# Kernel optimization log

Measured on AMD Instinct MI355X. Metric: run time of the kernel, lower is better.

Reference implementation:

```python
import jax, jax.numpy as jnp
import numpy as np

# db4 decomposition low-pass filter (pywt convention, 8 taps)
DEC_LO = np.array([-0.010597401784997278, 0.032883011666982945, 0.030841381835986965,
                   -0.18703481171888114, -0.02798376941698385, 0.6308807679295904,
                   0.7148465705525415, 0.23037781330885523], dtype=np.float32)
L = DEC_LO.shape[0]  # 8
REC_LO = DEC_LO[::-1].copy()
DEC_HI = (REC_LO * ((-1.0) ** (np.arange(L) + 1))).astype(np.float32)
REC_HI = DEC_HI[::-1].copy()
LEVEL = 7

# lax.conv does correlation; flip filters to get true convolution (pywt semantics)
K_DEC = jnp.asarray(np.stack([DEC_LO[::-1], DEC_HI[::-1]])[:, None, :])  # [2,1,L] out-ch: (lo, hi)
K_REC = jnp.asarray(np.stack([REC_LO[::-1], REC_HI[::-1]])[None, :, :])  # [1,2,L] in-ch: (ca, cd)


def dwt(x):
    # x: [B, N]. pywt zero-mode dwt == full conv then take odd indices;
    # fused here as stride-2 conv with asymmetric padding (L-2, L-1).
    y = jax.lax.conv_general_dilated(x[:, None, :], K_DEC, (2,), [(L - 2, L - 1)])
    return y[:, 0], y[:, 1]  # each [B, floor((N+L-1)/2)]


def idwt(ca, cd):
    # upsample-by-2 (lhs_dilation, length 2n-1), full conv, trim L-2 each side -> pad (1,1)
    y = jax.lax.conv_general_dilated(jnp.stack([ca, cd], axis=1), K_REC, (1,),
                                     [(1, 1)], lhs_dilation=(2,))
    return y[:, 0]  # [B, 2n - L + 2]


def soft(c, t):
    # pywt.threshold(mode='soft')
    return jnp.sign(c) * jnp.maximum(jnp.abs(c) - t, 0.0)


def setup_inputs() -> dict:
    key = jax.random.key(0)
    k1, k2 = jax.random.split(key)
    x = jax.random.normal(k1, (32768, 1116), dtype=jnp.float32)
    # learned scalar parameter, initialized like nn.Parameter(torch.tensor(0.02))
    raw_threshold = jnp.asarray(0.02, dtype=jnp.float32)
    return {"x": x, "raw_threshold": raw_threshold}


def reference(x, raw_threshold):
    thr = jnp.maximum(raw_threshold, 0.01)  # torch.clamp(min=0.01)
    # wavedec: 7-level analysis
    a = x
    details = []
    for _ in range(LEVEL):
        a, d = dwt(a)
        details.append(d)
    # soft-threshold every coefficient band (including approximation)
    a = soft(a, thr)
    details = [soft(d, thr) for d in details]
    # waverec: synthesis, truncating cA when one sample longer than cD (pywt rule)
    for d in reversed(details):
        if a.shape[-1] > d.shape[-1]:
            a = a[:, : d.shape[-1]]
        a = idwt(a, d)
    return a  # [B, 1116]
```

## Files before the change

### kernel.cpp

```cpp
#include <hip/hip_runtime.h>

#define NCOL 1116
#define NLEV 7
#define NT 256
#define RPB 4
#define ARENA 2048

static __device__ __forceinline__ float softf(float c, float t) {
    return copysignf(fmaxf(fabsf(c) - t, 0.0f), c);
}

__global__ __launch_bounds__(NT)
void wavelet_kernel(const float* __restrict__ x,
                    const float* __restrict__ thr_ptr,
                    float* __restrict__ out, int nrow) {
    constexpr float DEC_LO[8] = {-0.010597401784997278f,  0.032883011666982945f,
                                  0.030841381835986965f, -0.18703481171888114f,
                                 -0.02798376941698385f,   0.6308807679295904f,
                                  0.7148465705525415f,    0.23037781330885523f};
    constexpr float DEC_HI[8] = {-0.23037781330885523f,   0.7148465705525415f,
                                 -0.6308807679295904f,   -0.02798376941698385f,
                                  0.18703481171888114f,   0.030841381835986965f,
                                 -0.032883011666982945f, -0.010597401784997278f};
    constexpr float REC_LO[8] = { 0.23037781330885523f,   0.7148465705525415f,
                                  0.6308807679295904f,   -0.02798376941698385f,
                                 -0.18703481171888114f,   0.030841381835986965f,
                                  0.032883011666982945f, -0.010597401784997278f};
    constexpr float REC_HI[8] = {-0.010597401784997278f, -0.032883011666982945f,
                                  0.030841381835986965f,  0.18703481171888114f,
                                 -0.02798376941698385f,  -0.6308807679295904f,
                                  0.7148465705525415f,   -0.23037781330885523f};

    constexpr int alen[8] = {1116, 561, 284, 145, 76, 41, 24, 15};
    constexpr int doff[7] = {0, 562, 846, 992, 1068, 1110, 1134};

    __shared__ __align__(16) float SH[RPB * ARENA];

    const int lane = threadIdx.x & 63;
    const int wv   = threadIdx.x >> 6;
    const int row  = blockIdx.x * RPB + wv;
    if (row >= nrow) return;

    const float thr = fmaxf(thr_ptr[0], 0.01f);

    float* const arena = SH + wv * ARENA;
    float* const dpool = arena;
    float* const b8    = arena + 1156;
    float* const c8    = arena + 1732;

    {
        const float* xrow = x + (size_t)row * NCOL;
        #pragma unroll
        for (int k = 0; k < 9; ++k) {
            const int o = lane + (k << 6);
            if (o < 561) {
                float v[8];
                if (o >= 3 && o <= 557) {
                    const float2* p = (const float2*)(xrow + 2 * o - 6);
                    float2 q0 = p[0], q1 = p[1], q2 = p[2], q3 = p[3];
                    v[0] = q0.x; v[1] = q0.y; v[2] = q1.x; v[3] = q1.y;
                    v[4] = q2.x; v[5] = q2.y; v[6] = q3.x; v[7] = q3.y;
                } else {
                    #pragma unroll
                    for (int j = 0; j < 8; ++j) {
                        const int idx = 2 * o - 6 + j;
                        v[j] = (idx >= 0 && idx < NCOL) ? xrow[idx] : 0.0f;
                    }
                }
                float lo = 0.0f, hi = 0.0f;
                #pragma unroll
                for (int s = 0; s < 8; ++s) {
                    lo = fmaf(DEC_LO[s], v[7 - s], lo);
                    hi = fmaf(DEC_HI[s], v[7 - s], hi);
                }
                b8[o]    = lo;
                dpool[o] = softf(hi, thr);
            }
        }
        if (lane < 14) { const int j = lane < 6 ? lane - 6 : 555 + lane; b8[j] = 0.0f; }
        __builtin_amdgcn_wave_barrier();
    }

    #pragma unroll
    for (int l = 1; l < NLEV; ++l) {
        const int nout = alen[l + 1];
        float* const cur = (l & 1) ? b8 : c8;
        float* const nxt = (l & 1) ? c8 : b8;
        float* const dp  = dpool + doff[l];
        const int K = (nout + 63) >> 6;
        #pragma unroll
        for (int k = 0; k < K; ++k) {
            const int o = lane + (k << 6);
            if (o < nout) {
                const float2* p = (const float2*)(cur + 2 * o - 6);
                float2 q0 = p[0], q1 = p[1], q2 = p[2], q3 = p[3];
                float v[8];
                v[0] = q0.x; v[1] = q0.y; v[2] = q1.x; v[3] = q1.y;
                v[4] = q2.x; v[5] = q2.y; v[6] = q3.x; v[7] = q3.y;
                float lo = 0.0f, hi = 0.0f;
                #pragma unroll
                for (int s = 0; s < 8; ++s) {
                    lo = fmaf(DEC_LO[s], v[7 - s], lo);
                    hi = fmaf(DEC_HI[s], v[7 - s], hi);
                }
                nxt[o] = (l == NLEV - 1) ? softf(lo, thr) : lo;
                dp[o]  = softf(hi, thr);
            }
        }
        if (l < NLEV - 1 && lane < 14) {
            const int j = lane < 6 ? lane - 6 : nout + lane - 6;
            nxt[j] = 0.0f;
        }
        __builtin_amdgcn_wave_barrier();
    }

    #pragma unroll
    for (int l = NLEV - 1; l >= 1; --l) {
        const int M = alen[l + 1];
        const int npair = M - 3;
        const float* const cur = (l & 1) ? c8 : b8;
        float* const nxt       = (l & 1) ? b8 : c8;
        const float* const dp  = dpool + doff[l];
        const int KI = (((npair + 1) >> 1) + 63) >> 6;
        #pragma unroll
        for (int kk = 0; kk < KI; ++kk) {
            const int m = (lane + (kk << 6)) << 1;
            if (m < npair) {
                float ca[5], cd[5];
                #pragma unroll
                for (int j = 0; j < 5; ++j) { ca[j] = cur[m + j]; cd[j] = dp[m + j]; }
                float y0 = fmaf(REC_LO[0], ca[3], fmaf(REC_LO[2], ca[2], fmaf(REC_LO[4], ca[1], REC_LO[6] * ca[0])));
                y0 = fmaf(REC_HI[0], cd[3], fmaf(REC_HI[2], cd[2], fmaf(REC_HI[4], cd[1], fmaf(REC_HI[6], cd[0], y0))));
                float y1 = fmaf(REC_LO[1], ca[3], fmaf(REC_LO[3], ca[2], fmaf(REC_LO[5], ca[1], REC_LO[7] * ca[0])));
                y1 = fmaf(REC_HI[1], cd[3], fmaf(REC_HI[3], cd[2], fmaf(REC_HI[5], cd[1], fmaf(REC_HI[7], cd[0], y1))));
                if (m + 1 < npair) {
                    float y2 = fmaf(REC_LO[0], ca[4], fmaf(REC_LO[2], ca[3], fmaf(REC_LO[4], ca[2], REC_LO[6] * ca[1])));
                    y2 = fmaf(REC_HI[0], cd[4], fmaf(REC_HI[2], cd[3], fmaf(REC_HI[4], cd[2], fmaf(REC_HI[6], cd[1], y2))));
                    float y3 = fmaf(REC_LO[1], ca[4], fmaf(REC_LO[3], ca[3], fmaf(REC_LO[5], ca[2], REC_LO[7] * ca[1])));
                    y3 = fmaf(REC_HI[1], cd[4], fmaf(REC_HI[3], cd[3], fmaf(REC_HI[5], cd[2], fmaf(REC_HI[7], cd[1], y3))));
                    *(float4*)(nxt + 2 * m) = make_float4(y0, y1, y2, y3);
                } else {
                    nxt[2 * m]     = y0;
                    nxt[2 * m + 1] = y1;
                }
            }
        }
        __builtin_amdgcn_wave_barrier();
    }

    {
        const float* const cur = b8;
        const float* const dp  = dpool;
        float4* orow = (float4*)(out + (size_t)row * NCOL);
        #pragma unroll
        for (int kk = 0; kk < 5; ++kk) {
            const int bq = lane + (kk << 6);
            const int m = bq << 1;
            if (m < 558) {
                float ca[5], cd[5];
                #pragma unroll
                for (int j = 0; j < 5; ++j) { ca[j] = cur[m + j]; cd[j] = dp[m + j]; }
                float y0 = fmaf(REC_LO[0], ca[3], fmaf(REC_LO[2], ca[2], fmaf(REC_LO[4], ca[1], REC_LO[6] * ca[0])));
                y0 = fmaf(REC_HI[0], cd[3], fmaf(REC_HI[2], cd[2], fmaf(REC_HI[4], cd[1], fmaf(REC_HI[6], cd[0], y0))));
                float y1 = fmaf(REC_LO[1], ca[3], fmaf(REC_LO[3], ca[2], fmaf(REC_LO[5], ca[1], REC_LO[7] * ca[0])));
                y1 = fmaf(REC_HI[1], cd[3], fmaf(REC_HI[3], cd[2], fmaf(REC_HI[5], cd[1], fmaf(REC_HI[7], cd[0], y1))));
                float y2 = fmaf(REC_LO[0], ca[4], fmaf(REC_LO[2], ca[3], fmaf(REC_LO[4], ca[2], REC_LO[6] * ca[1])));
                y2 = fmaf(REC_HI[0], cd[4], fmaf(REC_HI[2], cd[3], fmaf(REC_HI[4], cd[2], fmaf(REC_HI[6], cd[1], y2))));
                float y3 = fmaf(REC_LO[1], ca[4], fmaf(REC_LO[3], ca[3], fmaf(REC_LO[5], ca[2], REC_LO[7] * ca[1])));
                y3 = fmaf(REC_HI[1], cd[4], fmaf(REC_HI[3], cd[3], fmaf(REC_HI[5], cd[2], fmaf(REC_HI[7], cd[1], y3))));
                orow[bq] = make_float4(y0, y1, y2, y3);
            }
        }
    }
}

extern "C" void kernel_launch(void* const* d_in, const int* in_sizes, int n_in,
                              void* d_out, int out_size, void* d_ws, size_t ws_size,
                              hipStream_t stream) {
    const float* x = (const float*)d_in[0];
    const float* thr = (const float*)d_in[1];
    float* out = (float*)d_out;
    const int nrow = in_sizes[0] / NCOL;
    const int nblk = (nrow + RPB - 1) / RPB;
    hipLaunchKernelGGL(wavelet_kernel, dim3(nblk), dim3(NT), 0, stream, x, thr, out, nrow);
}
```

Measured before the change: 254.3 us.

## Process two rows per single-wave block with interleaved per-row work

Blocks shrink to one 64-lane wave, and each wave handles two rows at once, interleaving their loads and filter math to raise instruction-level parallelism and hide LDS and global latency. Tail predicates become compile-time per-iteration masks, and synthesis reads use float2 LDS loads with a lane-0 epilogue for odd pair counts. This roughly doubles live registers per thread and halves the number of waves, which may lower occupancy. The last row is duplicated when nrow is odd.

```diff
diff --git a/kernel.cpp b/kernel.cpp
--- a/kernel.cpp
+++ b/kernel.cpp
@@ -2,114 +2,143 @@
 
 #define NCOL 1116
 #define NLEV 7
-#define NT 256
-#define RPB 4
+#define NT 64
 #define ARENA 2048
+#define NRPW 2
+
+namespace {
+constexpr float DEC_LO[8] = {-0.010597401784997278f,  0.032883011666982945f,
+                              0.030841381835986965f, -0.18703481171888114f,
+                             -0.02798376941698385f,   0.6308807679295904f,
+                              0.7148465705525415f,    0.23037781330885523f};
+constexpr float DEC_HI[8] = {-0.23037781330885523f,   0.7148465705525415f,
+                             -0.6308807679295904f,   -0.02798376941698385f,
+                              0.18703481171888114f,   0.030841381835986965f,
+                             -0.032883011666982945f, -0.010597401784997278f};
+constexpr float REC_LO[8] = { 0.23037781330885523f,   0.7148465705525415f,
+                              0.6308807679295904f,   -0.02798376941698385f,
+                             -0.18703481171888114f,   0.030841381835986965f,
+                              0.032883011666982945f, -0.010597401784997278f};
+constexpr float REC_HI[8] = {-0.010597401784997278f, -0.032883011666982945f,
+                              0.030841381835986965f,  0.18703481171888114f,
+                             -0.02798376941698385f,  -0.6308807679295904f,
+                              0.7148465705525415f,   -0.23037781330885523f};
+constexpr int alen[8] = {1116, 561, 284, 145, 76, 41, 24, 15};
+constexpr int doff[7] = {0, 562, 846, 992, 1068, 1110, 1134};
+}
 
 static __device__ __forceinline__ float softf(float c, float t) {
     return copysignf(fmaxf(fabsf(c) - t, 0.0f), c);
+}
+
+static __device__ __forceinline__ void dec8(const float* v, float& lo, float& hi) {
+    float l = DEC_LO[7] * v[0];
+    float h = DEC_HI[7] * v[0];
+    #pragma unroll
+    for (int s = 6; s >= 0; --s) {
+        l = fmaf(DEC_LO[s], v[7 - s], l);
+        h = fmaf(DEC_HI[s], v[7 - s], h);
+    }
+    lo = l; hi = h;
+}
+
+static __device__ __forceinline__ float2 rec_pair(float ca0, float ca1, float ca2, float ca3,
+                                                  float cd0, float cd1, float cd2, float cd3) {
+    float y0 = fmaf(REC_LO[0], ca3, fmaf(REC_LO[2], ca2, fmaf(REC_LO[4], ca1, REC_LO[6] * ca0)));
+    y0 = fmaf(REC_HI[0], cd3, fmaf(REC_HI[2], cd2, fmaf(REC_HI[4], cd1, fmaf(REC_HI[6], cd0, y0))));
+    float y1 = fmaf(REC_LO[1], ca3, fmaf(REC_LO[3], ca2, fmaf(REC_LO[5], ca1, REC_LO[7] * ca0)));
+    y1 = fmaf(REC_HI[1], cd3, fmaf(REC_HI[3], cd2, fmaf(REC_HI[5], cd1, fmaf(REC_HI[7], cd0, y1))));
+    return make_float2(y0, y1);
 }
 
 __global__ __launch_bounds__(NT)
 void wavelet_kernel(const float* __restrict__ x,
                     const float* __restrict__ thr_ptr,
                     float* __restrict__ out, int nrow) {
-    constexpr float DEC_LO[8] = {-0.010597401784997278f,  0.032883011666982945f,
-                                  0.030841381835986965f, -0.18703481171888114f,
-                                 -0.02798376941698385f,   0.6308807679295904f,
-                                  0.7148465705525415f,    0.23037781330885523f};
-    constexpr float DEC_HI[8] = {-0.23037781330885523f,   0.7148465705525415f,
-                                 -0.6308807679295904f,   -0.02798376941698385f,
-                                  0.18703481171888114f,   0.030841381835986965f,
-                                 -0.032883011666982945f, -0.010597401784997278f};
-    constexpr float REC_LO[8] = { 0.23037781330885523f,   0.7148465705525415f,
-                                  0.6308807679295904f,   -0.02798376941698385f,
-                                 -0.18703481171888114f,   0.030841381835986965f,
-                                  0.032883011666982945f, -0.010597401784997278f};
-    constexpr float REC_HI[8] = {-0.010597401784997278f, -0.032883011666982945f,
-                                  0.030841381835986965f,  0.18703481171888114f,
-                                 -0.02798376941698385f,  -0.6308807679295904f,
-                                  0.7148465705525415f,   -0.23037781330885523f};
-
-    constexpr int alen[8] = {1116, 561, 284, 145, 76, 41, 24, 15};
-    constexpr int doff[7] = {0, 562, 846, 992, 1068, 1110, 1134};
-
-    __shared__ __align__(16) float SH[RPB * ARENA];
-
-    const int lane = threadIdx.x & 63;
-    const int wv   = threadIdx.x >> 6;
-    const int row  = blockIdx.x * RPB + wv;
-    if (row >= nrow) return;
+    __shared__ __align__(16) float SH[NRPW * ARENA];
+
+    const int lane = threadIdx.x;
+    const int row0 = blockIdx.x * NRPW;
+    if (row0 >= nrow) return;
+    const int rows[2] = {row0, min(row0 + 1, nrow - 1)};
 
     const float thr = fmaxf(thr_ptr[0], 0.01f);
 
-    float* const arena = SH + wv * ARENA;
-    float* const dpool = arena;
-    float* const b8    = arena + 1156;
-    float* const c8    = arena + 1732;
+    float* dpool[NRPW]; float* b8[NRPW]; float* c8[NRPW];
+    #pragma unroll
+    for (int r = 0; r < NRPW; ++r) {
+        float* a = SH + r * ARENA;
+        dpool[r] = a;
+        b8[r]    = a + 1156;
+        c8[r]    = a + 1732;
+    }
 
     {
-        const float* xrow = x + (size_t)row * NCOL;
+        const float* xr[NRPW] = {x + (size_t)rows[0] * NCOL, x + (size_t)rows[1] * NCOL};
         #pragma unroll
         for (int k = 0; k < 9; ++k) {
             const int o = lane + (k << 6);
-            if (o < 561) {
-                float v[8];
-                if (o >= 3 && o <= 557) {
-                    const float2* p = (const float2*)(xrow + 2 * o - 6);
-                    float2 q0 = p[0], q1 = p[1], q2 = p[2], q3 = p[3];
-                    v[0] = q0.x; v[1] = q0.y; v[2] = q1.x; v[3] = q1.y;
-                    v[4] = q2.x; v[5] = q2.y; v[6] = q3.x; v[7] = q3.y;
-                } else {
-                    #pragma unroll
-                    for (int j = 0; j < 8; ++j) {
-                        const int idx = 2 * o - 6 + j;
-                        v[j] = (idx >= 0 && idx < NCOL) ? xrow[idx] : 0.0f;
+            if (k < 8 || lane < 49) {
+                #pragma unroll
+                for (int r = 0; r < NRPW; ++r) {
+                    float v[8];
+                    bool fast = (k >= 1 && k <= 7);
+                    if (!fast) fast = (o >= 3 && o <= 557);
+                    if (fast) {
+                        const float2* p = (const float2*)(xr[r] + 2 * o - 6);
+                        float2 q0 = p[0], q1 = p[1], q2 = p[2], q3 = p[3];
+                        v[0] = q0.x; v[1] = q0.y; v[2] = q1.x; v[3] = q1.y;
+                        v[4] = q2.x; v[5] = q2.y; v[6] = q3.x; v[7] = q3.y;
+                    } else {
+                        #pragma unroll
+                        for (int j = 0; j < 8; ++j) {
+                            const int idx = 2 * o - 6 + j;
+                            v[j] = (idx >= 0 && idx < NCOL) ? xr[r][idx] : 0.0f;
+                        }
                     }
-                }
-                float lo = 0.0f, hi = 0.0f;
-                #pragma unroll
-                for (int s = 0; s < 8; ++s) {
-                    lo = fmaf(DEC_LO[s], v[7 - s], lo);
-                    hi = fmaf(DEC_HI[s], v[7 - s], hi);
-                }
-                b8[o]    = lo;
-                dpool[o] = softf(hi, thr);
-            }
-        }
-        if (lane < 14) { const int j = lane < 6 ? lane - 6 : 555 + lane; b8[j] = 0.0f; }
+                    float lo, hi;
+                    dec8(v, lo, hi);
+                    b8[r][o]    = lo;
+                    dpool[r][o] = softf(hi, thr);
+                }
+            }
+        }
+        #pragma unroll
+        for (int r = 0; r < NRPW; ++r)
+            if (lane < 14) { const int j = lane < 6 ? lane - 6 : 555 + lane; b8[r][j] = 0.0f; }
         __builtin_amdgcn_wave_barrier();
     }
 
     #pragma unroll
     for (int l = 1; l < NLEV; ++l) {
         const int nout = alen[l + 1];
-        float* const cur = (l & 1) ? b8 : c8;
-        float* const nxt = (l & 1) ? c8 : b8;
-        float* const dp  = dpool + doff[l];
         const int K = (nout + 63) >> 6;
+        const int tailn = nout - ((K - 1) << 6);
         #pragma unroll
         for (int k = 0; k < K; ++k) {
             const int o = lane + (k << 6);
-            if (o < nout) {
-                const float2* p = (const float2*)(cur + 2 * o - 6);
-                float2 q0 = p[0], q1 = p[1], q2 = p[2], q3 = p[3];
-                float v[8];
-                v[0] = q0.x; v[1] = q0.y; v[2] = q1.x; v[3] = q1.y;
-                v[4] = q2.x; v[5] = q2.y; v[6] = q3.x; v[7] = q3.y;
-                float lo = 0.0f, hi = 0.0f;
-                #pragma unroll
-                for (int s = 0; s < 8; ++s) {
-                    lo = fmaf(DEC_LO[s], v[7 - s], lo);
-                    hi = fmaf(DEC_HI[s], v[7 - s], hi);
-                }
-                nxt[o] = (l == NLEV - 1) ? softf(lo, thr) : lo;
-                dp[o]  = softf(hi, thr);
-            }
-        }
-        if (l < NLEV - 1 && lane < 14) {
-            const int j = lane < 6 ? lane - 6 : nout + lane - 6;
-            nxt[j] = 0.0f;
+            if (k < K - 1 || lane < tailn) {
+                #pragma unroll
+                for (int r = 0; r < NRPW; ++r) {
+                    float* const cur = (l & 1) ? b8[r] : c8[r];
+                    float* const nxt = (l & 1) ? c8[r] : b8[r];
+                    const float2* p = (const float2*)(cur + 2 * o - 6);
+                    float2 q0 = p[0], q1 = p[1], q2 = p[2], q3 = p[3];
+                    float v[8] = {q0.x, q0.y, q1.x, q1.y, q2.x, q2.y, q3.x, q3.y};
+                    float lo, hi;
+                    dec8(v, lo, hi);
+                    nxt[o] = (l == NLEV - 1) ? softf(lo, thr) : lo;
+                    (dpool[r] + doff[l])[o] = softf(hi, thr);
+                }
+            }
+        }
+        if (l < NLEV - 1) {
+            #pragma unroll
+            for (int r = 0; r < NRPW; ++r)
+                if (lane < 14) {
+                    const int j = lane < 6 ? lane - 6 : nout + lane - 6;
+                    ((l & 1) ? c8[r] : b8[r])[j] = 0.0f;
+                }
         }
         __builtin_amdgcn_wave_barrier();
     }
@@ -118,57 +147,66 @@
     for (int l = NLEV - 1; l >= 1; --l) {
         const int M = alen[l + 1];
         const int npair = M - 3;
-        const float* const cur = (l & 1) ? c8 : b8;
-        float* const nxt       = (l & 1) ? b8 : c8;
-        const float* const dp  = dpool + doff[l];
-        const int KI = (((npair + 1) >> 1) + 63) >> 6;
-        #pragma unroll
-        for (int kk = 0; kk < KI; ++kk) {
-            const int m = (lane + (kk << 6)) << 1;
-            if (m < npair) {
-                float ca[5], cd[5];
-                #pragma unroll
-                for (int j = 0; j < 5; ++j) { ca[j] = cur[m + j]; cd[j] = dp[m + j]; }
-                float y0 = fmaf(REC_LO[0], ca[3], fmaf(REC_LO[2], ca[2], fmaf(REC_LO[4], ca[1], REC_LO[6] * ca[0])));
-                y0 = fmaf(REC_HI[0], cd[3], fmaf(REC_HI[2], cd[2], fmaf(REC_HI[4], cd[1], fmaf(REC_HI[6], cd[0], y0))));
-                float y1 = fmaf(REC_LO[1], ca[3], fmaf(REC_LO[3], ca[2], fmaf(REC_LO[5], ca[1], REC_LO[7] * ca[0])));
-                y1 = fmaf(REC_HI[1], cd[3], fmaf(REC_HI[3], cd[2], fmaf(REC_HI[5], cd[1], fmaf(REC_HI[7], cd[0], y1))));
-                if (m + 1 < npair) {
-                    float y2 = fmaf(REC_LO[0], ca[4], fmaf(REC_LO[2], ca[3], fmaf(REC_LO[4], ca[2], REC_LO[6] * ca[1])));
-                    y2 = fmaf(REC_HI[0], cd[4], fmaf(REC_HI[2], cd[3], fmaf(REC_HI[4], cd[2], fmaf(REC_HI[6], cd[1], y2))));
-                    float y3 = fmaf(REC_LO[1], ca[4], fmaf(REC_LO[3], ca[3], fmaf(REC_LO[5], ca[2], REC_LO[7] * ca[1])));
-                    y3 = fmaf(REC_HI[1], cd[4], fmaf(REC_HI[3], cd[3], fmaf(REC_HI[5], cd[2], fmaf(REC_HI[7], cd[1], y3))));
-                    *(float4*)(nxt + 2 * m) = make_float4(y0, y1, y2, y3);
-                } else {
-                    nxt[2 * m]     = y0;
-                    nxt[2 * m + 1] = y1;
-                }
+        const int Qf = npair >> 1;
+        const int KI = (Qf + 63) >> 6;
+        const int tailq = Qf - ((KI - 1) << 6);
+        #pragma unroll
+        for (int k = 0; k < KI; ++k) {
+            const int q = lane + (k << 6);
+            if (k < KI - 1 || lane < tailq) {
+                const int m = q << 1;
+                #pragma unroll
+                for (int r = 0; r < NRPW; ++r) {
+                    const float* const cur = (l & 1) ? c8[r] : b8[r];
+                    float* const nxt       = (l & 1) ? b8[r] : c8[r];
+                    const float* const dp  = dpool[r] + doff[l];
+                    const float2* pa = (const float2*)(cur + m);
+                    const float2* pd = (const float2*)(dp + m);
+                    float2 a01 = pa[0], a23 = pa[1];
+                    float2 d01 = pd[0], d23 = pd[1];
+                    float ca4 = cur[m + 4], cd4 = dp[m + 4];
+                    float2 y01 = rec_pair(a01.x, a01.y, a23.x, a23.y, d01.x, d01.y, d23.x, d23.y);
+                    float2 y23 = rec_pair(a01.y, a23.x, a23.y, ca4, d01.y, d23.x, d23.y, cd4);
+                    *(float4*)(nxt + 2 * m) = make_float4(y01.x, y01.y, y23.x, y23.y);
+                }
+            }
+        }
+        if ((npair & 1) && lane == 0) {
+            const int m = npair - 1;
+            #pragma unroll
+            for (int r = 0; r < NRPW; ++r) {
+                const float* const cur = (l & 1) ? c8[r] : b8[r];
+                float* const nxt       = (l & 1) ? b8[r] : c8[r];
+                const float* const dp  = dpool[r] + doff[l];
+                float2 y01 = rec_pair(cur[m], cur[m + 1], cur[m + 2], cur[m + 3],
+                                      dp[m],  dp[m + 1],  dp[m + 2],  dp[m + 3]);
+                *(float2*)(nxt + 2 * m) = y01;
             }
         }
         __builtin_amdgcn_wave_barrier();
     }
 
     {
-        const float* const cur = b8;
-        const float* const dp  = dpool;
-        float4* orow = (float4*)(out + (size_t)row * NCOL);
-        #pragma unroll
-        for (int kk = 0; kk < 5; ++kk) {
-            const int bq = lane + (kk << 6);
-            const int m = bq << 1;
-            if (m < 558) {
-                float ca[5], cd[5];
-                #pragma unroll
-                for (int j = 0; j < 5; ++j) { ca[j] = cur[m + j]; cd[j] = dp[m + j]; }
-                float y0 = fmaf(REC_LO[0], ca[3], fmaf(REC_LO[2], ca[2], fmaf(REC_LO[4], ca[1], REC_LO[6] * ca[0])));
-                y0 = fmaf(REC_HI[0], cd[3], fmaf(REC_HI[2], cd[2], fmaf(REC_HI[4], cd[1], fmaf(REC_HI[6], cd[0], y0))));
-                float y1 = fmaf(REC_LO[1], ca[3], fmaf(REC_LO[3], ca[2], fmaf(REC_LO[5], ca[1], REC_LO[7] * ca[0])));
-                y1 = fmaf(REC_HI[1], cd[3], fmaf(REC_HI[3], cd[2], fmaf(REC_HI[5], cd[1], fmaf(REC_HI[7], cd[0], y1))));
-                float y2 = fmaf(REC_LO[0], ca[4], fmaf(REC_LO[2], ca[3], fmaf(REC_LO[4], ca[2], REC_LO[6] * ca[1])));
-                y2 = fmaf(REC_HI[0], cd[4], fmaf(REC_HI[2], cd[3], fmaf(REC_HI[4], cd[2], fmaf(REC_HI[6], cd[1], y2))));
-                float y3 = fmaf(REC_LO[1], ca[4], fmaf(REC_LO[3], ca[3], fmaf(REC_LO[5], ca[2], REC_LO[7] * ca[1])));
-                y3 = fmaf(REC_HI[1], cd[4], fmaf(REC_HI[3], cd[3], fmaf(REC_HI[5], cd[2], fmaf(REC_HI[7], cd[1], y3))));
-                orow[bq] = make_float4(y0, y1, y2, y3);
+        float4* orow[NRPW] = {(float4*)(out + (size_t)rows[0] * NCOL),
+                              (float4*)(out + (size_t)rows[1] * NCOL)};
+        #pragma unroll
+        for (int k = 0; k < 5; ++k) {
+            const int q = lane + (k << 6);
+            if (k < 4 || lane < 23) {
+                const int m = q << 1;
+                #pragma unroll
+                for (int r = 0; r < NRPW; ++r) {
+                    const float* const cur = b8[r];
+                    const float* const dp  = dpool[r];
+                    const float2* pa = (const float2*)(cur + m);
+                    const float2* pd = (const float2*)(dp + m);
+                    float2 a01 = pa[0], a23 = pa[1];
+                    float2 d01 = pd[0], d23 = pd[1];
+                    float ca4 = cur[m + 4], cd4 = dp[m + 4];
+                    float2 y01 = rec_pair(a01.x, a01.y, a23.x, a23.y, d01.x, d01.y, d23.x, d23.y);
+                    float2 y23 = rec_pair(a01.y, a23.x, a23.y, ca4, d01.y, d23.x, d23.y, cd4);
+                    orow[r][q] = make_float4(y01.x, y01.y, y23.x, y23.y);
+                }
             }
         }
     }
@@ -181,6 +219,6 @@
     const float* thr = (const float*)d_in[1];
     float* out = (float*)d_out;
     const int nrow = in_sizes[0] / NCOL;
-    const int nblk = (nrow + RPB - 1) / RPB;
+    const int nblk = (nrow + NRPW - 1) / NRPW;
     hipLaunchKernelGGL(wavelet_kernel, dim3(nblk), dim3(NT), 0, stream, x, thr, out, nrow);
 }
```

Result: slower. 283.8 us (+11.6%).
